# Performance work log

Measured on AMD Instinct MI355X. Metric: run time of the kernel, lower is better.

## Reference

```python
import jax, jax.numpy as jnp
import numpy as np

ALPHA = 0.5  # distance-decay base (self.alpha)

def setup_inputs() -> dict:
    key = jax.random.key(0)
    N, E, D_IN, D_OUT = 50000, 800000, 128, 128
    k1, k2, k3, k4, k5 = jax.random.split(key, 5)
    h = jax.random.normal(k1, (N, D_IN), dtype=jnp.float32)
    # first N edges are self-loops so every node has in/out degree >= 1
    src = jnp.concatenate([jnp.arange(N), jax.random.randint(k2, (E - N,), 0, N)]).astype(jnp.int32)
    dst = jnp.concatenate([jnp.arange(N), jax.random.randint(k3, (E - N,), 0, N)]).astype(jnp.int32)
    distance = jax.random.randint(k4, (E,), 0, 6).astype(jnp.int32)
    limit = float(np.sqrt(6.0 / (D_IN + D_OUT)))  # xavier_uniform
    weight = jax.random.uniform(k5, (D_IN, D_OUT), jnp.float32, -limit, limit)
    bias = jnp.zeros((D_OUT,), jnp.float32)
    return {"h": h, "src": src, "dst": dst, "distance": distance, "weight": weight, "bias": bias}

def reference(h, src, dst, distance, weight, bias):
    N = h.shape[0]
    ones = jnp.ones(src.shape[0], jnp.float32)
    out_deg = jax.ops.segment_sum(ones, src, num_segments=N)  # [N]
    in_deg = jax.ops.segment_sum(ones, dst, num_segments=N)   # [N]
    # source-side symmetric norm
    feat = h * (out_deg ** -0.5)[:, None]                     # [N, D]
    # per-edge message: gathered src feature * alpha^distance
    w = jnp.power(jnp.float32(ALPHA), distance.astype(jnp.float32))  # [E]
    msg = feat[src] * w[:, None]                              # [E, D]
    # mean over mailbox == segment-sum / in-degree
    agg = jax.ops.segment_sum(msg, dst, num_segments=N) / in_deg[:, None]  # [N, D]
    rst = agg @ weight                                        # [N, D_OUT]
    rst = rst * (in_deg ** -0.5)[:, None] + bias
    return rst
```

## Files before the change

kernel.cpp:

```cpp
#include <hip/hip_runtime.h>


constexpr int D = 128;
constexpr int HC = 32;
constexpr int PNODES = 32;
constexpr int PCAP = 768;
constexpr int CHUNK = 8192;

typedef __attribute__((ext_vector_type(8))) short bf16x8;
typedef __attribute__((ext_vector_type(4))) float f32x4;

__device__ __forceinline__ float bf16_to_f(unsigned int u16) {
    union { unsigned int u; float f; } c; c.u = u16 << 16; return c.f;
}
__device__ __forceinline__ unsigned int f_to_bf16(float f) {
    union { float f; unsigned int u; } c; c.f = f;
    unsigned int u = c.u;
    u += 0x7fffu + ((u >> 16) & 1u);
    return u >> 16;
}

__global__ __launch_bounds__(256) void k_combo(const int* __restrict__ src,
        const int* __restrict__ dst, const int* __restrict__ dist,
        int* __restrict__ gcur, unsigned int* __restrict__ gbuf,
        unsigned int* __restrict__ slices,
        int E, int NW, int hchunk, int P, int nbA) {
    extern __shared__ int dyn[];
    int tid = threadIdx.x;

    if (blockIdx.x >= nbA) {
        unsigned int* bins = (unsigned int*)dyn;
        for (int i = tid; i < NW; i += 256) bins[i] = 0;
        __syncthreads();
        int c = blockIdx.x - nbA;
        int e0 = c * hchunk, e1 = min(e0 + hchunk, E);
        for (int i = e0 + tid * 4; i < e1; i += 1024) {
            if (i + 3 < e1) {
                int4 k4 = *(const int4*)&src[i];
                atomicAdd(&bins[k4.x >> 1], 1u << ((k4.x & 1) * 16));
                atomicAdd(&bins[k4.y >> 1], 1u << ((k4.y & 1) * 16));
                atomicAdd(&bins[k4.z >> 1], 1u << ((k4.z & 1) * 16));
                atomicAdd(&bins[k4.w >> 1], 1u << ((k4.w & 1) * 16));
            } else {
                for (int e = i; e < e1; e++)
                    atomicAdd(&bins[src[e] >> 1], 1u << ((src[e] & 1) * 16));
            }
        }
        __syncthreads();
        unsigned int* o = slices + (size_t)c * NW;
        for (int i = tid; i < NW; i += 256) o[i] = bins[i];
        return;
    }

    unsigned int* sorted = (unsigned int*)dyn;
    int* gidx  = dyn + CHUNK;
    int* hist  = dyn + 2 * CHUNK;
    int* start = hist + P;
    int* lofs  = start + P;
    int* base_g = lofs + P;
    __shared__ int wsum[4];

    int lane = tid & 63, w = tid >> 6;
    int e0 = blockIdx.x * CHUNK;
    int e1 = min(e0 + CHUNK, E);
    int ce = e1 - e0;

    for (int b = tid; b < P; b += 256) hist[b] = 0;
    __syncthreads();

    for (int i = e0 + tid * 4; i < e1; i += 1024) {
        if (i + 3 < e1) {
            int4 d4 = *(const int4*)&dst[i];
            atomicAdd(&hist[d4.x >> 5], 1);
            atomicAdd(&hist[d4.y >> 5], 1);
            atomicAdd(&hist[d4.z >> 5], 1);
            atomicAdd(&hist[d4.w >> 5], 1);
        } else {
            for (int e = i; e < e1; e++) atomicAdd(&hist[dst[e] >> 5], 1);
        }
    }
    __syncthreads();

    int loc[7];
    int s = 0;
    #pragma unroll
    for (int j = 0; j < 7; j++) {
        int b = tid * 7 + j;
        int v = (b < P) ? hist[b] : 0;
        loc[j] = s;
        s += v;
    }
    int x = s;
    #pragma unroll
    for (int off = 1; off < 64; off <<= 1) {
        int t = __shfl_up(x, off, 64);
        if (lane >= off) x += t;
    }
    if (lane == 63) wsum[w] = x;
    __syncthreads();
    int tbase = x - s;
    #pragma unroll
    for (int k = 0; k < 4; k++) if (k < w) tbase += wsum[k];
    #pragma unroll
    for (int j = 0; j < 7; j++) {
        int b = tid * 7 + j;
        if (b < P) {
            int st = tbase + loc[j];
            start[b] = st;
            lofs[b] = st;
            int cnt = hist[b];
            if (cnt) base_g[b] = atomicAdd(&gcur[b], cnt);
        }
    }
    __syncthreads();

    for (int i = e0 + tid * 4; i < e1; i += 1024) {
        if (i + 3 < e1) {
            int4 s4 = *(const int4*)&src[i];
            int4 d4 = *(const int4*)&dst[i];
            int4 q4 = *(const int4*)&dist[i];
            #pragma unroll
            for (int j = 0; j < 4; j++) {
                int sv = (&s4.x)[j], dv = (&d4.x)[j], qv = (&q4.x)[j];
                int p = dv >> 5;
                unsigned int wd = (unsigned)sv | ((unsigned)(dv & 31) << 16)
                                | ((unsigned)qv << 21);
                int pos = atomicAdd(&lofs[p], 1);
                sorted[pos] = wd;
                int rank = base_g[p] + (pos - start[p]);
                gidx[pos] = (rank < PCAP) ? p * PCAP + rank : -1;
            }
        } else {
            for (int e = i; e < e1; e++) {
                int sv = src[e], dv = dst[e], qv = dist[e];
                int p = dv >> 5;
                unsigned int wd = (unsigned)sv | ((unsigned)(dv & 31) << 16)
                                | ((unsigned)qv << 21);
                int pos = atomicAdd(&lofs[p], 1);
                sorted[pos] = wd;
                int rank = base_g[p] + (pos - start[p]);
                gidx[pos] = (rank < PCAP) ? p * PCAP + rank : -1;
            }
        }
    }
    __syncthreads();

    for (int i = tid; i < ce; i += 256) {
        int g = gidx[i];
        if (g >= 0) gbuf[g] = sorted[i];
    }
}

__global__ __launch_bounds__(256) void k_scale_cast(const unsigned int* __restrict__ slices,
        const float4* __restrict__ h4, uint4* __restrict__ hs4,
        const float* __restrict__ W, unsigned short* __restrict__ Wt,
        int N, int NW, int wblk) {
    if (blockIdx.x == wblk) {
        for (int i = threadIdx.x; i < D * D; i += 256) {
            int k = i >> 7, n = i & 127;
            Wt[n * D + k] = (unsigned short)f_to_bf16(W[i]);
        }
        return;
    }
    __shared__ float osc[256];
    int n0 = blockIdx.x * 256;
    int n = n0 + threadIdx.x;
    if (n < N) {
        int wi = n >> 1, sh = (n & 1) * 16;
        unsigned int s = 0;
        #pragma unroll 8
        for (int c = 0; c < HC; c++) s += slices[(size_t)c * NW + wi];
        osc[threadIdx.x] = rsqrtf((float)((s >> sh) & 0xffffu));
    }
    __syncthreads();
    int grp = threadIdx.x >> 4, lane = threadIdx.x & 15;
    int rend = min(256, N - n0);
    for (int r = grp; r < rend; r += 16) {
        int row = n0 + r;
        float sc = osc[r];
        float4 a = h4[(size_t)row * 32 + lane * 2];
        float4 b = h4[(size_t)row * 32 + lane * 2 + 1];
        uint4 o;
        o.x = f_to_bf16(a.x * sc) | (f_to_bf16(a.y * sc) << 16);
        o.y = f_to_bf16(a.z * sc) | (f_to_bf16(a.w * sc) << 16);
        o.z = f_to_bf16(b.x * sc) | (f_to_bf16(b.y * sc) << 16);
        o.w = f_to_bf16(b.z * sc) | (f_to_bf16(b.w * sc) << 16);
        hs4[(size_t)row * 16 + lane] = o;
    }
}

__global__ __launch_bounds__(256, 6) void k_pagg(const uint4* __restrict__ hs4,
        const unsigned int* __restrict__ gbuf, const int* __restrict__ gcur,
        const unsigned short* __restrict__ Wt, const float* __restrict__ bias,
        float* __restrict__ out, int N) {
    __shared__ unsigned int elist[PCAP];
    __shared__ unsigned int slist[PCAP];
    __shared__ int h2[PNODES], st2[PNODES], lo2[PNODES];
    __shared__ unsigned short As[PNODES * 136];
    int p = blockIdx.x;
    int tid = threadIdx.x;
    int cnt = min(gcur[p], PCAP);
    const unsigned int* gp = gbuf + (size_t)p * PCAP;

    if (tid < PNODES) h2[tid] = 0;
    __syncthreads();
    for (int i = tid; i < cnt; i += 256) {
        unsigned int wd = gp[i];
        elist[i] = wd;
        atomicAdd(&h2[(wd >> 16) & 31], 1);
    }
    __syncthreads();
    if (tid < 64) {
        int v = (tid < PNODES) ? h2[tid] : 0;
        int x = v;
        #pragma unroll
        for (int off = 1; off < 32; off <<= 1) {
            int t = __shfl_up(x, off, 64);
            if ((tid & 63) >= off) x += t;
        }
        if (tid < PNODES) { st2[tid] = x - v; lo2[tid] = x - v; }
    }
    __syncthreads();
    for (int i = tid; i < cnt; i += 256) {
        unsigned int wd = elist[i];
        int pos = atomicAdd(&lo2[(wd >> 16) & 31], 1);
        slist[pos] = wd;
    }
    __syncthreads();

    int wv = tid >> 6, l64 = tid & 63;
    int lane16 = l64 & 15, sub = l64 >> 4;
    #pragma unroll
    for (int k = 0; k < 8; k++) {
        int dl = wv * 8 + k;
        int node = p * PNODES + dl;
        int deg = h2[dl], b = st2[dl];
        float acc[8] = {0.f, 0.f, 0.f, 0.f, 0.f, 0.f, 0.f, 0.f};
        for (int eo = 0; eo < deg; eo += 16) {
            uint4 hv[4];
            float cc[4];
            #pragma unroll
            for (int j = 0; j < 4; j++) {
                int off = eo + j * 4 + sub;
                bool valid = off < deg;
                unsigned int wd = slist[b + (valid ? off : 0)];
                cc[j] = valid ? __uint_as_float((127u - ((wd >> 21) & 7u)) << 23)
                              : 0.f;
                hv[j] = hs4[(size_t)(wd & 0xffffu) * 16 + lane16];
            }
            #pragma unroll
            for (int j = 0; j < 4; j++) {
                float c = cc[j];
                acc[0] += c * bf16_to_f(hv[j].x & 0xffffu);
                acc[1] += c * bf16_to_f(hv[j].x >> 16);
                acc[2] += c * bf16_to_f(hv[j].y & 0xffffu);
                acc[3] += c * bf16_to_f(hv[j].y >> 16);
                acc[4] += c * bf16_to_f(hv[j].z & 0xffffu);
                acc[5] += c * bf16_to_f(hv[j].z >> 16);
                acc[6] += c * bf16_to_f(hv[j].w & 0xffffu);
                acc[7] += c * bf16_to_f(hv[j].w >> 16);
            }
        }
        #pragma unroll
        for (int j = 0; j < 8; j++) {
            acc[j] += __shfl_xor(acc[j], 16, 64);
            acc[j] += __shfl_xor(acc[j], 32, 64);
        }
        if (sub == 0) {
            uint4 o = make_uint4(0u, 0u, 0u, 0u);
            if (node < N) {
                float fd = (float)deg;
                float sc = rsqrtf(fd) / fd;
                o.x = f_to_bf16(acc[0] * sc) | (f_to_bf16(acc[1] * sc) << 16);
                o.y = f_to_bf16(acc[2] * sc) | (f_to_bf16(acc[3] * sc) << 16);
                o.z = f_to_bf16(acc[4] * sc) | (f_to_bf16(acc[5] * sc) << 16);
                o.w = f_to_bf16(acc[6] * sc) | (f_to_bf16(acc[7] * sc) << 16);
            }
            *(uint4*)&As[dl * 136 + lane16 * 8] = o;
        }
    }
    __syncthreads();

    int m = l64 & 15, quad = l64 >> 4;
    int mt = wv & 1, ntb = (wv >> 1) * 4;
    f32x4 acc2[4];
    #pragma unroll
    for (int t = 0; t < 4; t++) acc2[t] = (f32x4){0.f, 0.f, 0.f, 0.f};
    #pragma unroll
    for (int s = 0; s < 4; s++) {
        bf16x8 a = *(const bf16x8*)&As[(mt * 16 + m) * 136 + quad * 8 + s * 32];
        #pragma unroll
        for (int t = 0; t < 4; t++) {
            int n = (ntb + t) * 16 + m;
            bf16x8 b = *(const bf16x8*)&Wt[n * D + quad * 8 + s * 32];
            acc2[t] = __builtin_amdgcn_mfma_f32_16x16x32_bf16(a, b, acc2[t], 0, 0, 0);
        }
    }
    int orow0 = p * PNODES + mt * 16 + quad * 4;
    #pragma unroll
    for (int t = 0; t < 4; t++) {
        int n = (ntb + t) * 16 + m;
        float bz = bias[n];
        #pragma unroll
        for (int r = 0; r < 4; r++) {
            int grow = orow0 + r;
            if (grow < N) out[(size_t)grow * D + n] = acc2[t][r] + bz;
        }
    }
}

extern "C" void kernel_launch(void* const* d_in, const int* in_sizes, int n_in,
                              void* d_out, int out_size, void* d_ws, size_t ws_size,
                              hipStream_t stream) {
    const float* h    = (const float*)d_in[0];
    const int*   src  = (const int*)d_in[1];
    const int*   dst  = (const int*)d_in[2];
    const int*   dist = (const int*)d_in[3];
    const float* W    = (const float*)d_in[4];
    const float* bias = (const float*)d_in[5];
    float* out = (float*)d_out;
    const int N = in_sizes[0] / D;
    const int E = in_sizes[1];

    const int NW = (N + 1) / 2;
    const int hchunk = (((E + HC - 1) / HC) + 3) & ~3;
    const int P = (N + PNODES - 1) / PNODES;
    const int nbA = (E + CHUNK - 1) / CHUNK;

    char* ws = (char*)d_ws;
    size_t p = 0;
    auto alloc = [&](size_t bytes) -> char* {
        char* r = ws + p;
        p = (p + bytes + 511) & ~(size_t)511;
        return r;
    };
    unsigned int* slices = (unsigned int*)alloc((size_t)HC * NW * 4);
    int* gcur = (int*)alloc((size_t)P * 4);
    unsigned int* gbuf = (unsigned int*)alloc((size_t)P * PCAP * 4);
    unsigned short* hs = (unsigned short*)alloc((size_t)N * D * 2);
    unsigned short* Wt = (unsigned short*)alloc((size_t)D * D * 2);

    size_t dyn_part = ((size_t)2 * CHUNK + 4 * P) * 4;
    size_t dyn_hist = (size_t)NW * 4;
    size_t dyn_sz = dyn_part > dyn_hist ? dyn_part : dyn_hist;

    hipMemsetAsync(gcur, 0, (size_t)P * 4, stream);
    k_combo<<<nbA + HC, 256, dyn_sz, stream>>>(src, dst, dist, gcur, gbuf,
                                               slices, E, NW, hchunk, P, nbA);
    int nbsc = (N + 255) / 256;
    k_scale_cast<<<nbsc + 1, 256, 0, stream>>>(slices, (const float4*)h, (uint4*)hs,
                                               W, Wt, N, NW, nbsc);
    k_pagg<<<P, 256, 0, stream>>>((const uint4*)hs, gbuf, gcur, Wt, bias, out, N);
}
```

Baseline: 167.6 us.

## Fold scale-cast into combo kernel and apply out-degree norm per edge in aggregation

Removes the separate scale/cast kernel. The bf16 cast of h and the W transpose now run as extra blocks inside the partition/histogram kernel, so they overlap with edge bucketing. The out-degree histogram slices are merged with global atomics into one packed 16-bit-pair degree array instead of being written per slice and summed later. The rsqrt(out_deg) scaling moves into the aggregation kernel, where it is applied per edge through an extra gather of the degree. This saves one launch and the slice traffic, at the cost of global atomics and a per-edge degree load plus rsqrt in the hot loop.

```diff
diff --git a/kernel.cpp b/kernel.cpp
--- a/kernel.cpp
+++ b/kernel.cpp
@@ -6,6 +6,7 @@
 constexpr int PNODES = 32;
 constexpr int PCAP = 768;
 constexpr int CHUNK = 8192;
+constexpr int NCAST = 384;
 
 typedef __attribute__((ext_vector_type(8))) short bf16x8;
 typedef __attribute__((ext_vector_type(4))) float f32x4;
@@ -23,16 +24,42 @@
 __global__ __launch_bounds__(256) void k_combo(const int* __restrict__ src,
         const int* __restrict__ dst, const int* __restrict__ dist,
         int* __restrict__ gcur, unsigned int* __restrict__ gbuf,
-        unsigned int* __restrict__ slices,
-        int E, int NW, int hchunk, int P, int nbA) {
+        unsigned int* __restrict__ gdeg,
+        const float4* __restrict__ h4, uint4* __restrict__ hs4,
+        const float* __restrict__ W, unsigned short* __restrict__ Wt,
+        int E, int N, int NW, int hchunk, int P, int nbA) {
     extern __shared__ int dyn[];
     int tid = threadIdx.x;
-
-    if (blockIdx.x >= nbA) {
+    int bi = blockIdx.x;
+
+    if (bi >= nbA + HC) {
+        if (bi == nbA + HC) {
+            for (int i = tid; i < D * D; i += 256) {
+                int k = i >> 7, n = i & 127;
+                Wt[n * D + k] = (unsigned short)f_to_bf16(W[i]);
+            }
+            return;
+        }
+        int cb = bi - (nbA + HC + 1);
+        int G = N * (D / 8);
+        for (int i = cb * 256 + tid; i < G; i += NCAST * 256) {
+            float4 a = h4[2 * i];
+            float4 b = h4[2 * i + 1];
+            uint4 o;
+            o.x = f_to_bf16(a.x) | (f_to_bf16(a.y) << 16);
+            o.y = f_to_bf16(a.z) | (f_to_bf16(a.w) << 16);
+            o.z = f_to_bf16(b.x) | (f_to_bf16(b.y) << 16);
+            o.w = f_to_bf16(b.z) | (f_to_bf16(b.w) << 16);
+            hs4[i] = o;
+        }
+        return;
+    }
+
+    if (bi >= nbA) {
         unsigned int* bins = (unsigned int*)dyn;
         for (int i = tid; i < NW; i += 256) bins[i] = 0;
         __syncthreads();
-        int c = blockIdx.x - nbA;
+        int c = bi - nbA;
         int e0 = c * hchunk, e1 = min(e0 + hchunk, E);
         for (int i = e0 + tid * 4; i < e1; i += 1024) {
             if (i + 3 < e1) {
@@ -47,8 +74,10 @@
             }
         }
         __syncthreads();
-        unsigned int* o = slices + (size_t)c * NW;
-        for (int i = tid; i < NW; i += 256) o[i] = bins[i];
+        for (int i = tid; i < NW; i += 256) {
+            unsigned int v = bins[i];
+            if (v) atomicAdd(&gdeg[i], v);
+        }
         return;
     }
 
@@ -61,7 +90,7 @@
     __shared__ int wsum[4];
 
     int lane = tid & 63, w = tid >> 6;
-    int e0 = blockIdx.x * CHUNK;
+    int e0 = bi * CHUNK;
     int e1 = min(e0 + CHUNK, E);
     int ce = e1 - e0;
 
@@ -151,46 +180,9 @@
     }
 }
 
-__global__ __launch_bounds__(256) void k_scale_cast(const unsigned int* __restrict__ slices,
-        const float4* __restrict__ h4, uint4* __restrict__ hs4,
-        const float* __restrict__ W, unsigned short* __restrict__ Wt,
-        int N, int NW, int wblk) {
-    if (blockIdx.x == wblk) {
-        for (int i = threadIdx.x; i < D * D; i += 256) {
-            int k = i >> 7, n = i & 127;
-            Wt[n * D + k] = (unsigned short)f_to_bf16(W[i]);
-        }
-        return;
-    }
-    __shared__ float osc[256];
-    int n0 = blockIdx.x * 256;
-    int n = n0 + threadIdx.x;
-    if (n < N) {
-        int wi = n >> 1, sh = (n & 1) * 16;
-        unsigned int s = 0;
-        #pragma unroll 8
-        for (int c = 0; c < HC; c++) s += slices[(size_t)c * NW + wi];
-        osc[threadIdx.x] = rsqrtf((float)((s >> sh) & 0xffffu));
-    }
-    __syncthreads();
-    int grp = threadIdx.x >> 4, lane = threadIdx.x & 15;
-    int rend = min(256, N - n0);
-    for (int r = grp; r < rend; r += 16) {
-        int row = n0 + r;
-        float sc = osc[r];
-        float4 a = h4[(size_t)row * 32 + lane * 2];
-        float4 b = h4[(size_t)row * 32 + lane * 2 + 1];
-        uint4 o;
-        o.x = f_to_bf16(a.x * sc) | (f_to_bf16(a.y * sc) << 16);
-        o.y = f_to_bf16(a.z * sc) | (f_to_bf16(a.w * sc) << 16);
-        o.z = f_to_bf16(b.x * sc) | (f_to_bf16(b.y * sc) << 16);
-        o.w = f_to_bf16(b.z * sc) | (f_to_bf16(b.w * sc) << 16);
-        hs4[(size_t)row * 16 + lane] = o;
-    }
-}
-
 __global__ __launch_bounds__(256, 6) void k_pagg(const uint4* __restrict__ hs4,
         const unsigned int* __restrict__ gbuf, const int* __restrict__ gcur,
+        const unsigned short* __restrict__ gdeg16,
         const unsigned short* __restrict__ Wt, const float* __restrict__ bias,
         float* __restrict__ out, int N) {
     __shared__ unsigned int elist[PCAP];
@@ -244,9 +236,11 @@
                 int off = eo + j * 4 + sub;
                 bool valid = off < deg;
                 unsigned int wd = slist[b + (valid ? off : 0)];
-                cc[j] = valid ? __uint_as_float((127u - ((wd >> 21) & 7u)) << 23)
+                int sv = wd & 0xffff;
+                float os = rsqrtf((float)gdeg16[sv]);
+                cc[j] = valid ? __uint_as_float((127u - ((wd >> 21) & 7u)) << 23) * os
                               : 0.f;
-                hv[j] = hs4[(size_t)(wd & 0xffffu) * 16 + lane16];
+                hv[j] = hs4[(size_t)sv * 16 + lane16];
             }
             #pragma unroll
             for (int j = 0; j < 4; j++) {
@@ -334,8 +328,8 @@
         p = (p + bytes + 511) & ~(size_t)511;
         return r;
     };
-    unsigned int* slices = (unsigned int*)alloc((size_t)HC * NW * 4);
     int* gcur = (int*)alloc((size_t)P * 4);
+    unsigned int* gdeg = (unsigned int*)alloc((size_t)NW * 4);
     unsigned int* gbuf = (unsigned int*)alloc((size_t)P * PCAP * 4);
     unsigned short* hs = (unsigned short*)alloc((size_t)N * D * 2);
     unsigned short* Wt = (unsigned short*)alloc((size_t)D * D * 2);
@@ -344,11 +338,11 @@
     size_t dyn_hist = (size_t)NW * 4;
     size_t dyn_sz = dyn_part > dyn_hist ? dyn_part : dyn_hist;
 
-    hipMemsetAsync(gcur, 0, (size_t)P * 4, stream);
-    k_combo<<<nbA + HC, 256, dyn_sz, stream>>>(src, dst, dist, gcur, gbuf,
-                                               slices, E, NW, hchunk, P, nbA);
-    int nbsc = (N + 255) / 256;
-    k_scale_cast<<<nbsc + 1, 256, 0, stream>>>(slices, (const float4*)h, (uint4*)hs,
-                                               W, Wt, N, NW, nbsc);
-    k_pagg<<<P, 256, 0, stream>>>((const uint4*)hs, gbuf, gcur, Wt, bias, out, N);
-}
+    hipMemsetAsync(gcur, 0, (size_t)((char*)gdeg - (char*)gcur) + (size_t)NW * 4,
+                   stream);
+    k_combo<<<nbA + HC + 1 + NCAST, 256, dyn_sz, stream>>>(src, dst, dist,
+            gcur, gbuf, gdeg, (const float4*)h, (uint4*)hs, W, Wt,
+            E, N, NW, hchunk, P, nbA);
+    k_pagg<<<P, 256, 0, stream>>>((const uint4*)hs, gbuf, gcur,
+            (const unsigned short*)gdeg, Wt, bias, out, N);
+}
```

Measured after the change: 161.3 us. 3.8% less time.
